# Kernel optimization log

Measured on AMD Instinct MI355X. Metric: run time of the kernel, lower is better.

The kernel has to match this reference:

```python
import jax, jax.numpy as jnp
import numpy as np

NUM_EMBEDDINGS = 1024
EMBEDDING_DIM = 64
COMMITMENT_COST = 0.25


def setup_inputs() -> dict:
    key = jax.random.key(0)
    k1, k2 = jax.random.split(key)
    latents = jax.random.normal(k1, (64, EMBEDDING_DIM, 32, 32), dtype=jnp.float32)
    # torch init: uniform_(-1/num_embeddings, 1/num_embeddings)
    codebook = jax.random.uniform(
        k2, (NUM_EMBEDDINGS, EMBEDDING_DIM), dtype=jnp.float32,
        minval=-1.0 / NUM_EMBEDDINGS, maxval=1.0 / NUM_EMBEDDINGS)
    return {"latents": latents, "codebook": codebook}


def reference(latents, codebook):
    B, C, H, W = latents.shape
    K = codebook.shape[0]
    x = jnp.transpose(latents, (0, 2, 3, 1))            # [B,H,W,C]
    x_flat = x.reshape(-1, C)                            # [N,C]
    # squared euclidean distances [N,K]
    dist = (jnp.sum(x_flat ** 2, axis=1, keepdims=True)
            + jnp.sum(codebook ** 2, axis=1)
            - 2.0 * x_flat @ codebook.T)
    idx = jnp.argmin(dist, axis=1)                       # [N] int
    q_flat = codebook[idx]                               # [N,C]
    q = q_flat.reshape(x.shape)                          # [B,H,W,C]
    e_loss = jnp.mean((jax.lax.stop_gradient(q) - x) ** 2)
    q_loss = jnp.mean((q - jax.lax.stop_gradient(x)) ** 2)
    vq_loss = q_loss + COMMITMENT_COST * e_loss
    # straight-through estimator
    q_st = x + jax.lax.stop_gradient(q - x)
    quantized = jnp.transpose(q_st, (0, 3, 1, 2))        # [B,C,H,W]
    # perplexity from code usage histogram
    N = x_flat.shape[0]
    avg_probs = jnp.zeros((K,), dtype=jnp.float32).at[idx].add(1.0) / N
    perplexity = jnp.exp(-jnp.sum(avg_probs * jnp.log(avg_probs + 1e-10)))
    encoding_indices = idx.reshape(B, H, W)
    return (vq_loss, quantized, perplexity, encoding_indices)
```

## Files before the change

kernel.cpp:

```cpp
#include <hip/hip_runtime.h>

#define N_PTS   65536
#define K_CODES 1024
#define C_DIM   64
#define HW      1024
#define Q_ELEMS 4194304

#define OUT_Q_OFF 1
#define OUT_P_OFF 4194305
#define OUT_I_OFF 4194306

#define WS_HIST 0
#define WS_SSE  4096
#define WS_CSUM 8192
#define WS_CBP  16384

#define EPS_A_W 7.5e-5f
#define EPS_T_W 2.0e-4f

typedef float f32x16 __attribute__((ext_vector_type(16)));
typedef short bf16x8 __attribute__((ext_vector_type(8)));

__device__ __forceinline__ unsigned short bf16rn(float f) {
    unsigned int u = __float_as_uint(f);
    return (unsigned short)((u + 0x7FFFu + ((u >> 16) & 1u)) >> 16);
}
__device__ __forceinline__ float bf16tof(unsigned short h) {
    return __uint_as_float(((unsigned int)h) << 16);
}

__device__ __forceinline__ float np_pairwise_sumsq64(const float* a) {
    float r[8];
    #pragma unroll
    for (int j = 0; j < 8; ++j) r[j] = __fmul_rn(a[j], a[j]);
    #pragma unroll
    for (int i = 8; i < 64; i += 8) {
        #pragma unroll
        for (int j = 0; j < 8; ++j)
            r[j] = __fadd_rn(r[j], __fmul_rn(a[i + j], a[i + j]));
    }
    return __fadd_rn(__fadd_rn(__fadd_rn(r[0], r[1]), __fadd_rn(r[2], r[3])),
                     __fadd_rn(__fadd_rn(r[4], r[5]), __fadd_rn(r[6], r[7])));
}

__global__ void vq_prep(const float* __restrict__ cb, float* __restrict__ csum,
                        unsigned short* __restrict__ cbp) {
    int g = blockIdx.x * 256 + threadIdx.x;
    int t = g >> 6, lane = g & 63, l31 = lane & 31, half = lane >> 5;
    int row = t * 32 + l31;
    const float* r = cb + row * 64;
    float cs = np_pairwise_sumsq64(r);
    if (half == 0) csum[row] = cs;
    size_t tb = (size_t)t * 9 * 512;
    #pragma unroll
    for (int c = 0; c < 4; ++c) {
        bf16x8 h8, l8;
        #pragma unroll
        for (int j = 0; j < 8; ++j) {
            float f = r[c * 16 + half * 8 + j];
            unsigned short h = bf16rn(f);
            h8[j] = (short)h;
            l8[j] = (short)bf16rn(f - bf16tof(h));
        }
        *(bf16x8*)(cbp + tb + (size_t)(c * 2 + 0) * 512 + lane * 8) = h8;
        *(bf16x8*)(cbp + tb + (size_t)(c * 2 + 1) * 512 + lane * 8) = l8;
    }
    bf16x8 c8;
    #pragma unroll
    for (int j = 0; j < 8; ++j) c8[j] = 0;
    if (half == 0) c8[0] = (short)bf16rn(-0.5f * cs);
    *(bf16x8*)(cbp + tb + (size_t)8 * 512 + lane * 8) = c8;
}

__global__ __launch_bounds__(256, 2) void vq_main(
        const float* __restrict__ latents,
        const float* __restrict__ cb,
        const float* __restrict__ csum,
        const unsigned short* __restrict__ cbp,
        unsigned int* __restrict__ hist,
        double* __restrict__ sse,
        float* __restrict__ out) {
    __shared__ float xs[128 * 65];
    __shared__ float tmax[32 * 128];
    __shared__ float m1f[128];
    __shared__ int   fk[128], ambig[128], acount;
    __shared__ double dred[128];

    const int tid  = threadIdx.x;
    const int lane = tid & 63, wave = tid >> 6;
    const int n0 = blockIdx.x * 128;
    const int b = n0 >> 10, hw0 = n0 & 1023;
    const float* xg = latents + (size_t)b * C_DIM * HW + hw0;

    for (int i = tid; i < 128 * 64; i += 256) {
        int p = i & 127, d = i >> 7;
        xs[p * 65 + d] = xg[(size_t)d * HW + p];
    }
    if (tid == 0) acount = 0;
    __syncthreads();

    const int l31 = lane & 31, half = lane >> 5;
    const int pb = (wave << 5) + l31;
    bf16x8 xh[4], xl[4], x4;
    #pragma unroll
    for (int c = 0; c < 4; ++c)
        #pragma unroll
        for (int j = 0; j < 8; ++j) {
            float f = xs[pb * 65 + c * 16 + half * 8 + j];
            unsigned short h = bf16rn(f);
            xh[c][j] = (short)h;
            xl[c][j] = (short)bf16rn(f - bf16tof(h));
        }
    #pragma unroll
    for (int j = 0; j < 8; ++j) x4[j] = 0;
    if (half == 0) x4[0] = (short)0x3F80;

    float m1 = -3e38f, m2 = -3e38f;
    int i1 = 0;
    const int RC[16] = {0,1,2,3,8,9,10,11,16,17,18,19,24,25,26,27};
    const int rh4 = half * 4;
    const bf16x8* base = (const bf16x8*)cbp;

    auto screen_tile = [&](int t, const bf16x8* ch, const bf16x8* cl, bf16x8 ca) {
        f32x16 accA, accB;
        #pragma unroll
        for (int r = 0; r < 16; ++r) { accA[r] = 0.0f; accB[r] = 0.0f; }
        #pragma unroll
        for (int c = 0; c < 4; ++c)
            accA = __builtin_amdgcn_mfma_f32_32x32x16_bf16(ch[c], xh[c], accA, 0, 0, 0);
        accA = __builtin_amdgcn_mfma_f32_32x32x16_bf16(ca, x4, accA, 0, 0, 0);
        #pragma unroll
        for (int c = 0; c < 4; ++c)
            accB = __builtin_amdgcn_mfma_f32_32x32x16_bf16(ch[c], xl[c], accB, 0, 0, 0);
        #pragma unroll
        for (int c = 0; c < 4; ++c)
            accB = __builtin_amdgcn_mfma_f32_32x32x16_bf16(cl[c], xh[c], accB, 0, 0, 0);
        float tl = -3e38f;
        const int tb = t << 5;
        #pragma unroll
        for (int r = 0; r < 16; ++r) {
            float v = accA[r] + accB[r];
            int k = tb + RC[r] + rh4;
            m2 = fmaxf(m2, fminf(m1, v));
            i1 = (v > m1) ? k : i1;
            m1 = fmaxf(m1, v);
            tl = fmaxf(tl, v);
        }
        tl = fmaxf(tl, __shfl_xor(tl, 32, 64));
        if (half == 0) tmax[t * 128 + pb] = tl;
    };
    auto load_tile = [&](int t, bf16x8* ch, bf16x8* cl, bf16x8& ca) {
        const bf16x8* bp = base + (size_t)t * 576 + lane;
        #pragma unroll
        for (int c = 0; c < 4; ++c) {
            ch[c] = bp[c * 128];
            cl[c] = bp[c * 128 + 64];
        }
        ca = bp[512];
    };

    bf16x8 chA[4], clA[4], caA, chB[4], clB[4], caB;
    load_tile(0, chA, clA, caA);
    for (int t = 0; t < 32; t += 2) {
        load_tile(t + 1, chB, clB, caB);
        screen_tile(t, chA, clA, caA);
        if (t + 2 < 32) load_tile(t + 2, chA, clA, caA);
        screen_tile(t + 1, chB, clB, caB);
    }
    {
        float m1o = __shfl_xor(m1, 32, 64);
        float m2o = __shfl_xor(m2, 32, 64);
        int   i1o = __shfl_xor(i1, 32, 64);
        m2 = fmaxf(fmaxf(m2, m2o), fminf(m1, m1o));
        i1 = (m1o > m1) ? i1o : i1;
        m1 = fmaxf(m1, m1o);
        if (half == 0) {
            m1f[pb] = m1;
            fk[pb] = i1;
            if (m2 >= m1 - EPS_A_W) {
                int a = atomicAdd(&acount, 1);
                ambig[a] = pb;
            }
        }
    }
    __syncthreads();

    for (int a = wave; a < acount; a += 4) {
        int p = ambig[a];
        const float* xrow = &xs[p * 65];
        float Aq = np_pairwise_sumsq64(xrow);
        float thr = m1f[p] - EPS_T_W;
        unsigned long long best = ~0ULL;
        for (int t = 0; t < 32; ++t) {
            if (tmax[t * 128 + p] < thr) continue;
            if (lane < 32) {
                int k = (t << 5) + lane;
                const float* crow = cb + (size_t)k * 64;
                float m = 0.0f;
                #pragma unroll
                for (int d = 0; d < 64; ++d) m = __fmaf_rn(xrow[d], crow[d], m);
                float D = __fsub_rn(__fadd_rn(Aq, csum[k]), __fmul_rn(2.0f, m));
                unsigned long long key =
                    ((unsigned long long)__float_as_uint(D) << 10) | (unsigned)k;
                best = (key < best) ? key : best;
            }
        }
        #pragma unroll
        for (int off = 32; off > 0; off >>= 1) {
            unsigned long long o = __shfl_xor(best, off, 64);
            best = (o < best) ? o : best;
        }
        if (lane == 0) fk[p] = (int)(best & 1023ULL);
    }
    __syncthreads();

    if (tid < 128) {
        int myk = fk[tid];
        out[OUT_I_OFF + n0 + tid] = (float)myk;
        atomicAdd(&hist[myk], 1u);
        const float* crow = cb + (size_t)myk * 64;
        const float* xrow = &xs[tid * 65];
        double e = 0.0;
        #pragma unroll
        for (int d = 0; d < 64; ++d) {
            double df = (double)xrow[d] - (double)crow[d];
            e = fma(df, df, e);
        }
        dred[tid] = e;
    }
    __syncthreads();
    if (tid < 64) {
        double v = dred[tid] + dred[tid + 64];
        #pragma unroll
        for (int off = 32; off > 0; off >>= 1) v += __shfl_down(v, off, 64);
        if (tid == 0) atomicAdd(sse, v);
    }
    for (int i = tid; i < 128 * 64; i += 256) {
        int p = i & 127, c = i >> 7;
        out[OUT_Q_OFF + (size_t)b * 65536 + (size_t)c * HW + hw0 + p] =
            cb[(size_t)fk[p] * 64 + c];
    }
}

__global__ void vq_final(const unsigned int* __restrict__ hist,
                         const double* __restrict__ sse,
                         float* __restrict__ out) {
    __shared__ double red[256];
    int t = threadIdx.x;
    double s = 0.0;
    for (int i = t; i < K_CODES; i += 256) {
        double p = (double)hist[i] / (double)N_PTS;
        s += p * log(p + 1e-10);
    }
    red[t] = s;
    __syncthreads();
    for (int w = 128; w > 0; w >>= 1) {
        if (t < w) red[t] += red[t + w];
        __syncthreads();
    }
    if (t == 0) {
        out[OUT_P_OFF] = (float)exp(-red[0]);
        out[0] = (float)(1.25 * sse[0] / (double)Q_ELEMS);
    }
}

extern "C" void kernel_launch(void* const* d_in, const int* in_sizes, int n_in,
                              void* d_out, int out_size, void* d_ws, size_t ws_size,
                              hipStream_t stream) {
    const float* latents = (const float*)d_in[0];
    const float* cb      = (const float*)d_in[1];
    float* out = (float*)d_out;
    char* ws = (char*)d_ws;

    unsigned int*   hist = (unsigned int*)(ws + WS_HIST);
    double*         sse  = (double*)(ws + WS_SSE);
    float*          csum = (float*)(ws + WS_CSUM);
    unsigned short* cbp  = (unsigned short*)(ws + WS_CBP);

    hipMemsetAsync(ws, 0, 4096 + 8, stream);

    vq_prep <<<8, 256, 0, stream>>>(cb, csum, cbp);
    vq_main <<<N_PTS / 128, 256, 0, stream>>>(latents, cb, csum, cbp, hist, sse, out);
    vq_final<<<1, 256, 0, stream>>>(hist, sse, out);
}
```

Measured before the change: 141.3 us.

## Split codebook scan across wave pairs, fuse final reduction, drop memset

Doubles the block to 512 threads so each pair of waves scans half the codebook tiles for the same 32 points, then merges top-2 results through shared memory. The screen tile now uses a single accumulator chain and tracks a per-tile top-2 with med3. The per-point SSE and quantized gather become vectorised float4 reads staged in shared memory before a coalesced store. The memset and the final kernel are removed: prep zeroes the counters and the last block (via a done counter) computes perplexity and loss. The changes cut launch overhead and add parallelism, at the cost of a serial MFMA dependency chain and the extra cross-wave merge.

```diff
diff --git a/kernel.cpp b/kernel.cpp
--- a/kernel.cpp
+++ b/kernel.cpp
@@ -12,6 +12,7 @@
 
 #define WS_HIST 0
 #define WS_SSE  4096
+#define WS_DONE 4104
 #define WS_CSUM 8192
 #define WS_CBP  16384
 
@@ -44,8 +45,13 @@
 }
 
 __global__ void vq_prep(const float* __restrict__ cb, float* __restrict__ csum,
-                        unsigned short* __restrict__ cbp) {
+                        unsigned short* __restrict__ cbp,
+                        unsigned int* __restrict__ hist,
+                        double* __restrict__ sse,
+                        unsigned int* __restrict__ done) {
     int g = blockIdx.x * 256 + threadIdx.x;
+    if (g < 1024) hist[g] = 0u;
+    if (g == 1024) { *sse = 0.0; *done = 0u; }
     int t = g >> 6, lane = g & 63, l31 = lane & 31, half = lane >> 5;
     int row = t * 32 + l31;
     const float* r = cb + row * 64;
@@ -72,27 +78,32 @@
     *(bf16x8*)(cbp + tb + (size_t)8 * 512 + lane * 8) = c8;
 }
 
-__global__ __launch_bounds__(256, 2) void vq_main(
+__global__ __launch_bounds__(512, 4) void vq_main(
         const float* __restrict__ latents,
         const float* __restrict__ cb,
         const float* __restrict__ csum,
         const unsigned short* __restrict__ cbp,
         unsigned int* __restrict__ hist,
         double* __restrict__ sse,
+        unsigned int* __restrict__ done,
         float* __restrict__ out) {
     __shared__ float xs[128 * 65];
     __shared__ float tmax[32 * 128];
+    __shared__ float m1s[8 * 32], m2s[8 * 32];
+    __shared__ int   i1s[8 * 32];
     __shared__ float m1f[128];
     __shared__ int   fk[128], ambig[128], acount;
-    __shared__ double dred[128];
+    __shared__ double wred[8];
+    __shared__ int isLast;
 
     const int tid  = threadIdx.x;
     const int lane = tid & 63, wave = tid >> 6;
+    const int grp = wave >> 1, thalf = wave & 1;
     const int n0 = blockIdx.x * 128;
     const int b = n0 >> 10, hw0 = n0 & 1023;
     const float* xg = latents + (size_t)b * C_DIM * HW + hw0;
 
-    for (int i = tid; i < 128 * 64; i += 256) {
+    for (int i = tid; i < 128 * 64; i += 512) {
         int p = i & 127, d = i >> 7;
         xs[p * 65 + d] = xg[(size_t)d * HW + p];
     }
@@ -100,7 +111,7 @@
     __syncthreads();
 
     const int l31 = lane & 31, half = lane >> 5;
-    const int pb = (wave << 5) + l31;
+    const int pb = (grp << 5) + l31;
     bf16x8 xh[4], xl[4], x4;
     #pragma unroll
     for (int c = 0; c < 4; ++c)
@@ -121,34 +132,6 @@
     const int rh4 = half * 4;
     const bf16x8* base = (const bf16x8*)cbp;
 
-    auto screen_tile = [&](int t, const bf16x8* ch, const bf16x8* cl, bf16x8 ca) {
-        f32x16 accA, accB;
-        #pragma unroll
-        for (int r = 0; r < 16; ++r) { accA[r] = 0.0f; accB[r] = 0.0f; }
-        #pragma unroll
-        for (int c = 0; c < 4; ++c)
-            accA = __builtin_amdgcn_mfma_f32_32x32x16_bf16(ch[c], xh[c], accA, 0, 0, 0);
-        accA = __builtin_amdgcn_mfma_f32_32x32x16_bf16(ca, x4, accA, 0, 0, 0);
-        #pragma unroll
-        for (int c = 0; c < 4; ++c)
-            accB = __builtin_amdgcn_mfma_f32_32x32x16_bf16(ch[c], xl[c], accB, 0, 0, 0);
-        #pragma unroll
-        for (int c = 0; c < 4; ++c)
-            accB = __builtin_amdgcn_mfma_f32_32x32x16_bf16(cl[c], xh[c], accB, 0, 0, 0);
-        float tl = -3e38f;
-        const int tb = t << 5;
-        #pragma unroll
-        for (int r = 0; r < 16; ++r) {
-            float v = accA[r] + accB[r];
-            int k = tb + RC[r] + rh4;
-            m2 = fmaxf(m2, fminf(m1, v));
-            i1 = (v > m1) ? k : i1;
-            m1 = fmaxf(m1, v);
-            tl = fmaxf(tl, v);
-        }
-        tl = fmaxf(tl, __shfl_xor(tl, 32, 64));
-        if (half == 0) tmax[t * 128 + pb] = tl;
-    };
     auto load_tile = [&](int t, bf16x8* ch, bf16x8* cl, bf16x8& ca) {
         const bf16x8* bp = base + (size_t)t * 576 + lane;
         #pragma unroll
@@ -158,13 +141,47 @@
         }
         ca = bp[512];
     };
+    auto screen_tile = [&](int t, const bf16x8* ch, const bf16x8* cl, bf16x8 ca) {
+        f32x16 acc;
+        #pragma unroll
+        for (int r = 0; r < 16; ++r) acc[r] = 0.0f;
+        acc = __builtin_amdgcn_mfma_f32_32x32x16_bf16(ca, x4, acc, 0, 0, 0);
+        #pragma unroll
+        for (int c = 0; c < 4; ++c)
+            acc = __builtin_amdgcn_mfma_f32_32x32x16_bf16(ch[c], xh[c], acc, 0, 0, 0);
+        #pragma unroll
+        for (int c = 0; c < 4; ++c)
+            acc = __builtin_amdgcn_mfma_f32_32x32x16_bf16(ch[c], xl[c], acc, 0, 0, 0);
+        #pragma unroll
+        for (int c = 0; c < 4; ++c)
+            acc = __builtin_amdgcn_mfma_f32_32x32x16_bf16(cl[c], xh[c], acc, 0, 0, 0);
+        float vl = -3e38f, sl = -3e38f;
+        int kl = 0;
+        #pragma unroll
+        for (int r = 0; r < 16; ++r) {
+            float v = acc[r];
+            sl = __builtin_amdgcn_fmed3f(v, sl, vl);
+            bool c2 = v > vl;
+            kl = c2 ? RC[r] : kl;
+            vl = fmaxf(vl, v);
+        }
+        int k = (t << 5) + rh4 + kl;
+        bool cg = vl > m1;
+        i1 = cg ? k : i1;
+        float X = cg ? sl : m2;
+        m2 = __builtin_amdgcn_fmed3f(vl, X, m1);
+        m1 = fmaxf(m1, vl);
+        float tlm = fmaxf(vl, __shfl_xor(vl, 32, 64));
+        if (half == 0) tmax[t * 128 + pb] = tlm;
+    };
 
     bf16x8 chA[4], clA[4], caA, chB[4], clB[4], caB;
-    load_tile(0, chA, clA, caA);
-    for (int t = 0; t < 32; t += 2) {
+    const int t0 = thalf << 4;
+    load_tile(t0, chA, clA, caA);
+    for (int t = t0; t < t0 + 16; t += 2) {
         load_tile(t + 1, chB, clB, caB);
         screen_tile(t, chA, clA, caA);
-        if (t + 2 < 32) load_tile(t + 2, chA, clA, caA);
+        if (t + 2 < t0 + 16) load_tile(t + 2, chA, clA, caA);
         screen_tile(t + 1, chB, clB, caB);
     }
     {
@@ -175,17 +192,30 @@
         i1 = (m1o > m1) ? i1o : i1;
         m1 = fmaxf(m1, m1o);
         if (half == 0) {
-            m1f[pb] = m1;
-            fk[pb] = i1;
-            if (m2 >= m1 - EPS_A_W) {
-                int a = atomicAdd(&acount, 1);
-                ambig[a] = pb;
-            }
-        }
-    }
-    __syncthreads();
-
-    for (int a = wave; a < acount; a += 4) {
+            m1s[wave * 32 + l31] = m1;
+            m2s[wave * 32 + l31] = m2;
+            i1s[wave * 32 + l31] = i1;
+        }
+    }
+    __syncthreads();
+    if (tid < 128) {
+        int p = tid, l = p & 31, wA = (p >> 5) * 2;
+        float a1 = m1s[wA * 32 + l], a2 = m2s[wA * 32 + l];
+        float b1 = m1s[wA * 32 + 32 + l], b2 = m2s[wA * 32 + 32 + l];
+        int   ai = i1s[wA * 32 + l],  bi = i1s[wA * 32 + 32 + l];
+        bool cg = b1 > a1;
+        float mm1 = fmaxf(a1, b1);
+        float mm2 = __builtin_amdgcn_fmed3f(a1, b1, cg ? b2 : a2);
+        m1f[p] = mm1;
+        fk[p]  = cg ? bi : ai;
+        if (mm2 >= mm1 - EPS_A_W) {
+            int a = atomicAdd(&acount, 1);
+            ambig[a] = p;
+        }
+    }
+    __syncthreads();
+
+    for (int a = wave; a < acount; a += 8) {
         int p = ambig[a];
         const float* xrow = &xs[p * 65];
         float Aq = np_pairwise_sumsq64(xrow);
@@ -218,49 +248,62 @@
         int myk = fk[tid];
         out[OUT_I_OFF + n0 + tid] = (float)myk;
         atomicAdd(&hist[myk], 1u);
-        const float* crow = cb + (size_t)myk * 64;
-        const float* xrow = &xs[tid * 65];
-        double e = 0.0;
-        #pragma unroll
-        for (int d = 0; d < 64; ++d) {
-            double df = (double)xrow[d] - (double)crow[d];
-            e = fma(df, df, e);
-        }
-        dred[tid] = e;
-    }
-    __syncthreads();
-    if (tid < 64) {
-        double v = dred[tid] + dred[tid + 64];
-        #pragma unroll
-        for (int off = 32; off > 0; off >>= 1) v += __shfl_down(v, off, 64);
-        if (tid == 0) atomicAdd(sse, v);
-    }
-    for (int i = tid; i < 128 * 64; i += 256) {
+    }
+    double e = 0.0;
+    #pragma unroll
+    for (int i2 = 0; i2 < 4; ++i2) {
+        int i = tid + i2 * 512;
+        int p = i >> 4, seg = i & 15;
+        const float4 q = *(const float4*)(cb + (size_t)fk[p] * 64 + seg * 4);
+        float* xp = &xs[p * 65 + seg * 4];
+        float x0 = xp[0], x1 = xp[1], x2 = xp[2], x3 = xp[3];
+        double d0 = (double)x0 - (double)q.x; e = fma(d0, d0, e);
+        double d1 = (double)x1 - (double)q.y; e = fma(d1, d1, e);
+        double d2 = (double)x2 - (double)q.z; e = fma(d2, d2, e);
+        double d3 = (double)x3 - (double)q.w; e = fma(d3, d3, e);
+        xp[0] = q.x; xp[1] = q.y; xp[2] = q.z; xp[3] = q.w;
+    }
+    #pragma unroll
+    for (int off = 32; off > 0; off >>= 1) e += __shfl_down(e, off, 64);
+    if (lane == 0) wred[wave] = e;
+    __syncthreads();
+    if (tid == 0) {
+        double s = 0.0;
+        #pragma unroll
+        for (int w = 0; w < 8; ++w) s += wred[w];
+        atomicAdd(sse, s);
+    }
+    for (int i = tid; i < 128 * 64; i += 512) {
         int p = i & 127, c = i >> 7;
-        out[OUT_Q_OFF + (size_t)b * 65536 + (size_t)c * HW + hw0 + p] =
-            cb[(size_t)fk[p] * 64 + c];
-    }
-}
-
-__global__ void vq_final(const unsigned int* __restrict__ hist,
-                         const double* __restrict__ sse,
-                         float* __restrict__ out) {
-    __shared__ double red[256];
-    int t = threadIdx.x;
-    double s = 0.0;
-    for (int i = t; i < K_CODES; i += 256) {
-        double p = (double)hist[i] / (double)N_PTS;
-        s += p * log(p + 1e-10);
-    }
-    red[t] = s;
-    __syncthreads();
-    for (int w = 128; w > 0; w >>= 1) {
-        if (t < w) red[t] += red[t + w];
+        out[OUT_Q_OFF + (size_t)b * 65536 + (size_t)c * HW + hw0 + p] = xs[p * 65 + c];
+    }
+
+    __threadfence();
+    __syncthreads();
+    if (tid == 0)
+        isLast = (atomicAdd(done, 1u) == (unsigned)(gridDim.x - 1)) ? 1 : 0;
+    __syncthreads();
+    if (isLast) {
+        double s = 0.0;
+        for (int i = tid; i < K_CODES; i += 512) {
+            unsigned int h = __hip_atomic_load(&hist[i], __ATOMIC_RELAXED,
+                                               __HIP_MEMORY_SCOPE_AGENT);
+            double pr = (double)h / (double)N_PTS;
+            s += pr * log(pr + 1e-10);
+        }
+        #pragma unroll
+        for (int off = 32; off > 0; off >>= 1) s += __shfl_down(s, off, 64);
+        if (lane == 0) wred[wave] = s;
         __syncthreads();
-    }
-    if (t == 0) {
-        out[OUT_P_OFF] = (float)exp(-red[0]);
-        out[0] = (float)(1.25 * sse[0] / (double)Q_ELEMS);
+        if (tid == 0) {
+            double st = 0.0;
+            #pragma unroll
+            for (int w = 0; w < 8; ++w) st += wred[w];
+            double sv = __hip_atomic_load(sse, __ATOMIC_RELAXED,
+                                          __HIP_MEMORY_SCOPE_AGENT);
+            out[OUT_P_OFF] = (float)exp(-st);
+            out[0] = (float)(1.25 * sv / (double)Q_ELEMS);
+        }
     }
 }
 
@@ -274,12 +317,11 @@
 
     unsigned int*   hist = (unsigned int*)(ws + WS_HIST);
     double*         sse  = (double*)(ws + WS_SSE);
+    unsigned int*   done = (unsigned int*)(ws + WS_DONE);
     float*          csum = (float*)(ws + WS_CSUM);
     unsigned short* cbp  = (unsigned short*)(ws + WS_CBP);
 
-    hipMemsetAsync(ws, 0, 4096 + 8, stream);
-
-    vq_prep <<<8, 256, 0, stream>>>(cb, csum, cbp);
-    vq_main <<<N_PTS / 128, 256, 0, stream>>>(latents, cb, csum, cbp, hist, sse, out);
-    vq_final<<<1, 256, 0, stream>>>(hist, sse, out);
-}
+    vq_prep<<<8, 256, 0, stream>>>(cb, csum, cbp, hist, sse, done);
+    vq_main<<<N_PTS / 128, 512, 0, stream>>>(latents, cb, csum, cbp,
+                                             hist, sse, done, out);
+}
```

After: 331.2 us. +134.4%, slower.
